# Kernel optimization log

Hardware: AMD Instinct MI355X
Metric: run time of the kernel (lower is better)

## Reference

```python
import jax, jax.numpy as jnp
import numpy as np
import math

B, P, C, D, H = 4, 2048, 512, 1024, 16
DH = D // H
EPS = 1e-6


def setup_inputs() -> dict:
    key = jax.random.key(0)
    ks = jax.random.split(key, 10)
    para = jax.random.normal(ks[0], (B, P, D), dtype=jnp.float32)
    cluster = jax.random.normal(ks[1], (B, C, D), dtype=jnp.float32)
    e = jax.random.uniform(ks[2], (B, P, C), dtype=jnp.float32)
    edge = jnp.where(e > 0.5, e, 0.0)
    s = 1.0 / math.sqrt(D)
    Wq = jax.random.uniform(ks[3], (D, D), jnp.float32, -s, s)
    bq = jnp.zeros((D,), jnp.float32)
    Wk = jax.random.uniform(ks[4], (D, D), jnp.float32, -s, s)
    bk = jnp.zeros((D,), jnp.float32)
    Wv = jax.random.uniform(ks[5], (D, D), jnp.float32, -s, s)
    bv = jnp.zeros((D,), jnp.float32)
    gamma = jnp.ones((D,), jnp.float32)
    beta = jnp.zeros((D,), jnp.float32)
    return {"para": para, "cluster": cluster, "edge": edge,
            "Wq": Wq, "bq": bq, "Wk": Wk, "bk": bk, "Wv": Wv, "bv": bv,
            "gamma": gamma, "beta": beta}


def reference(para, cluster, edge, Wq, bq, Wk, bk, Wv, bv, gamma, beta):
    # projections: [B, L, D] -> [B, H, L, DH]
    def shape(x):
        b, l, _ = x.shape
        return x.reshape(b, l, H, DH).transpose(0, 2, 1, 3)

    q = shape(para @ Wq + bq) / math.sqrt(DH)   # [B,H,P,DH]
    k = shape(cluster @ Wk + bk)                # [B,H,C,DH]
    v = shape(cluster @ Wv + bv)                # [B,H,C,DH]

    scores = jnp.einsum('bhpd,bhcd->bhpc', q, k)  # [B,H,P,C]
    mask = (edge > 0)[:, None, :, :]              # broadcast over heads
    scores = jnp.where(mask, scores, -1e18)
    attn = jax.nn.softmax(scores, axis=-1)
    attn = attn * edge[:, None, :, :]             # post-softmax edge weighting
    # dropout is identity at inference
    ctx = jnp.einsum('bhpc,bhcd->bhpd', attn, v)  # [B,H,P,DH]
    ctx = ctx.transpose(0, 2, 1, 3).reshape(B, P, D)
    # LayerNorm(model_dim), eps=1e-6
    mu = jnp.mean(ctx, axis=-1, keepdims=True)
    var = jnp.mean(jnp.square(ctx - mu), axis=-1, keepdims=True)
    out = (ctx - mu) * jax.lax.rsqrt(var + EPS) * gamma + beta
    return out
```

## Files before the change

### kernel.cpp

```cpp
#include <hip/hip_runtime.h>

#define BB 4
#define PP 2048
#define CCLUS 512
#define DD 1024
#define HH 16
#define DHH 64

typedef __attribute__((ext_vector_type(8))) short short8;
typedef __attribute__((ext_vector_type(4))) float floatx4;
typedef unsigned short u16;
typedef unsigned int u32;
typedef unsigned long long u64;

__device__ __forceinline__ float bf2f(u16 u) {
  union { u32 i; float f; } v; v.i = ((u32)u) << 16; return v.f;
}
__device__ __forceinline__ u16 f2bf(float f) {
  union { float f; u32 i; } v; v.f = f;
  u32 x = v.i;
  return (u16)((x + 0x7fffu + ((x >> 16) & 1u)) >> 16);
}
__device__ __forceinline__ u64 pack4(float a, float b, float c, float d) {
  return (u64)f2bf(a) | ((u64)f2bf(b) << 16) | ((u64)f2bf(c) << 32) | ((u64)f2bf(d) << 48);
}

__device__ __forceinline__ floatx4 mfma16(short8 a, short8 b, floatx4 c) {
  return __builtin_amdgcn_mfma_f32_16x16x32_bf16(a, b, c, 0, 0, 0);
}

__device__ __forceinline__ void gload_lds16(const u16* g, u16* l) {
  __builtin_amdgcn_global_load_lds(
      (const __attribute__((address_space(1))) u32*)g,
      (__attribute__((address_space(3))) u32*)l, 16, 0, 0);
}

__global__ __launch_bounds__(256) void prep_k(
    const float* __restrict__ para, const float* __restrict__ cluster,
    const float* __restrict__ Wq, const float* __restrict__ Wk, const float* __restrict__ Wv,
    u16* __restrict__ Ap, u16* __restrict__ Ac,
    u16* __restrict__ WqT, u16* __restrict__ WkT, u16* __restrict__ WvT) {
  const int tid = threadIdx.x;
  if (blockIdx.x < 3072) {
    __shared__ u16 tile[32][33];
    const int job = blockIdx.x;
    const int z = job >> 10;
    const int t = job & 1023;
    const int bx = t & 31, by = t >> 5;
    const float* src = (z == 0) ? Wq : (z == 1) ? Wk : Wv;
    u16* dst = (z == 0) ? WqT : (z == 1) ? WkT : WvT;
    const int c = tid & 31, r0 = tid >> 5;
#pragma unroll
    for (int rr = 0; rr < 4; rr++) {
      const int row = r0 + rr * 8;
      tile[row][c] = f2bf(src[(size_t)(by * 32 + row) * DD + bx * 32 + c]);
    }
    __syncthreads();
#pragma unroll
    for (int rr = 0; rr < 4; rr++) {
      const int row = r0 + rr * 8;
      dst[(size_t)(bx * 32 + row) * DD + by * 32 + c] = tile[c][row];
    }
  } else {
    const int NP4 = (BB * PP * DD) / 4;
    const int NC4 = (BB * CCLUS * DD) / 4;
    const int stride = 1024 * 256;
    for (int i = (blockIdx.x - 3072) * 256 + tid; i < NP4 + NC4; i += stride) {
      const float* src; u16* dst; int j;
      if (i < NP4) { src = para; dst = Ap; j = i; }
      else         { src = cluster; dst = Ac; j = i - NP4; }
      const float4 v = *(const float4*)(src + (size_t)j * 4);
      *(u64*)(dst + (size_t)j * 4) = pack4(v.x, v.y, v.z, v.w);
    }
  }
}

__global__ __launch_bounds__(256) void qkv_gemm5(
    const u16* __restrict__ Ap, const u16* __restrict__ Ac,
    const u16* __restrict__ WqT, const u16* __restrict__ WkT, const u16* __restrict__ WvT,
    const float* __restrict__ bq, const float* __restrict__ bk, const float* __restrict__ bv,
    u16* __restrict__ Qb, u16* __restrict__ Kp, u16* __restrict__ Vt) {
  const int bx = blockIdx.x;
  const u16* A; const u16* BT; const float* bias; float scale; int mt, mode;
  if (bx < 64)      { A = Ap; BT = WqT; bias = bq; scale = 0.18033688f; mt = bx;      mode = 0; }
  else if (bx < 80) { A = Ac; BT = WkT; bias = bk; scale = 1.0f;        mt = bx - 64; mode = 1; }
  else              { A = Ac; BT = WvT; bias = bv; scale = 1.0f;        mt = bx - 80; mode = 2; }

  __shared__ __align__(16) u16 SH[16384];
  u16* As = SH;
  u16* Bs = SH + 4096;
  u16* T2 = SH;

  const int tid = threadIdx.x;
  const int w = tid >> 6, lane = tid & 63, quad = lane >> 4, cidx = lane & 15;
  const int wy = w >> 1, wx = w & 1;
  const int m0 = mt * 128, n0 = blockIdx.y * 128;

  floatx4 acc[4][4];
#pragma unroll
  for (int i = 0; i < 4; i++)
#pragma unroll
    for (int j = 0; j < 4; j++) acc[i][j] = (floatx4){0.f, 0.f, 0.f, 0.f};

  const int row0 = tid >> 2, kc0 = tid & 3;
  const int offG0 = row0 * 1024 + kc0 * 8;
  const int offG1 = (row0 + 64) * 1024 + kc0 * 8;
  u16* ldsA0 = As + (size_t)(w * 64) * 8;
  u16* ldsA1 = As + (size_t)(w * 64 + 256) * 8;
  u16* ldsB0 = Bs + (size_t)(w * 64) * 8;
  u16* ldsB1 = Bs + (size_t)(w * 64 + 256) * 8;

  const u16* Abase = A + (size_t)m0 * 1024;
  const u16* Bbase = BT + (size_t)n0 * 1024;

  for (int kt = 0; kt < 32; kt++) {
    const u16* Ak = Abase + kt * 32;
    const u16* Bk = Bbase + kt * 32;
    gload_lds16(Ak + offG0, ldsA0);
    gload_lds16(Ak + offG1, ldsA1);
    gload_lds16(Bk + offG0, ldsB0);
    gload_lds16(Bk + offG1, ldsB1);
    __syncthreads();

    short8 af[4], bfr[4];
#pragma unroll
    for (int i = 0; i < 4; i++) {
      int ra = wy * 64 + i * 16 + cidx;
      af[i] = *(const short8*)&As[ra * 32 + quad * 8];
      int rb = wx * 64 + i * 16 + cidx;
      bfr[i] = *(const short8*)&Bs[rb * 32 + quad * 8];
    }
#pragma unroll
    for (int mi = 0; mi < 4; mi++)
#pragma unroll
      for (int ni = 0; ni < 4; ni++)
        acc[mi][ni] = mfma16(af[mi], bfr[ni], acc[mi][ni]);
    __syncthreads();
  }

  if (mode != 2) {
#pragma unroll
    for (int ni = 0; ni < 4; ni++) {
      const int ncol = n0 + wx * 64 + ni * 16 + cidx;
      const float bvv = bias[ncol];
#pragma unroll
      for (int mi = 0; mi < 4; mi++) {
        const int mrow = m0 + wy * 64 + mi * 16 + quad * 4;
        if (mode == 1) {
          const int hh2 = ncol >> 6, dh = ncol & 63;
#pragma unroll
          for (int r = 0; r < 4; r++) {
            const int row = mrow + r;
            const int bb = row >> 9, c = row & 511;
            Kp[((size_t)(bb * HH + hh2) * CCLUS + c) * DHH + dh] = f2bf(acc[mi][ni][r] + bvv);
          }
        } else {
#pragma unroll
          for (int r = 0; r < 4; r++) {
            float v = (acc[mi][ni][r] + bvv) * scale;
            Qb[(size_t)(mrow + r) * 1024 + ncol] = f2bf(v);
          }
        }
      }
    }
  } else {
    const int b = m0 >> 9;
    const int c0g = m0 & 511;
    const int h0g = n0 >> 6;
#pragma unroll
    for (int p = 0; p < 2; p++) {
      if (wx == p) {
#pragma unroll
        for (int ni = 0; ni < 4; ni++) {
          const int col = ni * 16 + cidx;
          const float bvv = bias[n0 + wx * 64 + col];
          const int swzv = (col & 7) << 3;
#pragma unroll
          for (int mi = 0; mi < 4; mi++) {
            const int rowb = wy * 64 + mi * 16 + quad * 4;
            *(u64*)&T2[col * 128 + (rowb ^ swzv)] =
                pack4(acc[mi][ni][0] + bvv, acc[mi][ni][1] + bvv,
                      acc[mi][ni][2] + bvv, acc[mi][ni][3] + bvv);
          }
        }
      }
      __syncthreads();
      {
        const int col = tid >> 2, quarter = tid & 3;
        const int swzv = (col & 7) << 3;
        u16* vrow = Vt + ((size_t)(b * HH + h0g + p) * 64 + col) * 512 + c0g + quarter * 32;
#pragma unroll
        for (int j = 0; j < 4; j++) {
          const short8 vv = *(const short8*)&T2[col * 128 + ((quarter * 32 + j * 8) ^ swzv)];
          *(short8*)(vrow + j * 8) = vv;
        }
      }
      __syncthreads();
    }
  }
}

__global__ __launch_bounds__(512, 8) void attn_k5(
    const u16* __restrict__ Qb, const u16* __restrict__ Kp, const u16* __restrict__ Vt,
    const float* __restrict__ edge, float* __restrict__ ctx) {
  const int b = blockIdx.z, h = blockIdx.y, p0 = blockIdx.x * 128;
  const int tid = threadIdx.x;
  const int w = tid >> 6, lane = tid & 63, quad = lane >> 4, cidx = lane & 15;

  __shared__ __align__(16) u16 Ks[2][64 * 64];
  __shared__ __align__(16) u16 Vs[2][64 * 64];

  const u16* __restrict__ Kbh = Kp + (size_t)(b * HH + h) * CCLUS * DHH;
  const u16* __restrict__ Vbh = Vt + (size_t)(b * HH + h) * DHH * CCLUS;

  const int prow = p0 + w * 16 + cidx;
  const u16* qg = Qb + (size_t)(b * PP + prow) * DD + h * DHH + quad * 8;
  const short8 qf0 = *(const short8*)qg;
  const short8 qf1 = *(const short8*)(qg + 32);
  const float* Erow = edge + (size_t)(b * PP + prow) * CCLUS;

  float srow = 0.f;
  floatx4 oacc[4];
#pragma unroll
  for (int nt = 0; nt < 4; nt++) oacc[nt] = (floatx4){0.f, 0.f, 0.f, 0.f};

  const int srow_i = tid >> 3;
  const int sc = ((tid & 7) ^ (srow_i & 7)) << 3;
  const int ldsoff = w * 512;

  auto STAGE = [&](int cc, int bufi) {
    const u16* kg = Kbh + (size_t)cc * 64 * DHH;
    const u16* vg = Vbh + cc * 64;
    gload_lds16(kg + (size_t)srow_i * DHH + sc, &Ks[bufi][ldsoff]);
    gload_lds16(vg + (size_t)srow_i * CCLUS + sc, &Vs[bufi][ldsoff]);
  };

  STAGE(0, 0);
  __syncthreads();

  const int swz = (cidx & 7) << 3;

  for (int cc = 0; cc < 8; cc++) {
    const int bufi = cc & 1;
    if (cc < 7) STAGE(cc + 1, bufi ^ 1);
    const u16* __restrict__ KsB = &Ks[bufi][0];
    const u16* __restrict__ VsB = &Vs[bufi][0];

#pragma unroll
    for (int ks = 0; ks < 2; ks++) {
      u32 pa[2], pb[2];
#pragma unroll
      for (int tt = 0; tt < 2; tt++) {
        const int t = ks * 2 + tt;
        const int krow = (t * 16 + cidx) * 64;
        const short8 kf0 = *(const short8*)&KsB[krow + ((quad * 8) ^ swz)];
        const short8 kf1 = *(const short8*)&KsB[krow + ((32 + quad * 8) ^ swz)];
        floatx4 s4 = (floatx4){0.f, 0.f, 0.f, 0.f};
        __builtin_amdgcn_s_setprio(1);
        s4 = mfma16(kf0, qf0, s4);
        s4 = mfma16(kf1, qf1, s4);
        __builtin_amdgcn_s_setprio(0);
        const int ce = cc * 64 + t * 16 + quad * 4;
        const float4 e4 = *(const float4*)(Erow + ce);
        float E[4];
#pragma unroll
        for (int r = 0; r < 4; r++) {
          const float e = (&e4.x)[r];
          float x = fminf(s4[r], 21.6f);
          float ex;
          asm("v_exp_f32 %0, %1\n\ts_nop 0" : "=v"(ex) : "v"(x));
          ex = (e > 0.f) ? ex : 0.f;
          srow += ex;
          E[r] = ex * e;
        }
        asm("v_cvt_pk_bf16_f32 %0, %1, %2" : "=v"(pa[tt]) : "v"(E[0]), "v"(E[1]));
        asm("v_cvt_pk_bf16_f32 %0, %1, %2" : "=v"(pb[tt]) : "v"(E[2]), "v"(E[3]));
      }
      asm("v_permlane32_swap_b32 %0, %1" : "+v"(pa[0]), "+v"(pa[1]));
      asm("v_permlane16_swap_b32 %0, %1" : "+v"(pa[0]), "+v"(pa[1]));
      asm("v_permlane32_swap_b32 %0, %1" : "+v"(pb[0]), "+v"(pb[1]));
      asm("v_permlane16_swap_b32 %0, %1" : "+v"(pb[0]), "+v"(pb[1]));
      union { u32 u[4]; short8 s; } af;
      af.u[0] = pa[0]; af.u[1] = pb[0]; af.u[2] = pa[1]; af.u[3] = pb[1];
      __builtin_amdgcn_s_setprio(1);
#pragma unroll
      for (int nt = 0; nt < 4; nt++) {
        const short8 bfr =
            *(const short8*)&VsB[(nt * 16 + cidx) * 64 + ((ks * 32 + quad * 8) ^ swz)];
        oacc[nt] = mfma16(af.s, bfr, oacc[nt]);
      }
      __builtin_amdgcn_s_setprio(0);
    }
    __syncthreads();
  }

  srow += __shfl_xor(srow, 16, 64);
  srow += __shfl_xor(srow, 32, 64);
  const float sinv = (srow > 0.f) ? 1.0f / srow : 0.f;

#pragma unroll
  for (int r = 0; r < 4; r++) {
    const float sv = __shfl(sinv, quad * 4 + r, 16);
#pragma unroll
    for (int nt = 0; nt < 4; nt++) {
      const size_t off =
          (size_t)(b * PP + p0 + w * 16 + quad * 4 + r) * DD + h * DHH + nt * 16 + cidx;
      ctx[off] = oacc[nt][r] * sv;
    }
  }
}

__global__ __launch_bounds__(256) void ln_k(
    float* buf, const float* __restrict__ gamma, const float* __restrict__ beta) {
  const int row = blockIdx.x, tid = threadIdx.x;
  const int w = tid >> 6, lane = tid & 63;
  float* x = buf + (size_t)row * DD + tid * 4;
  float4 v = *(const float4*)x;
  float s = v.x + v.y + v.z + v.w;
  float sq = v.x * v.x + v.y * v.y + v.z * v.z + v.w * v.w;
#pragma unroll
  for (int off = 1; off < 64; off <<= 1) {
    s += __shfl_xor(s, off, 64);
    sq += __shfl_xor(sq, off, 64);
  }
  __shared__ float red[8];
  if (lane == 0) { red[w] = s; red[4 + w] = sq; }
  __syncthreads();
  s = red[0] + red[1] + red[2] + red[3];
  sq = red[4] + red[5] + red[6] + red[7];
  const float mu = s * (1.f / 1024.f);
  const float var = sq * (1.f / 1024.f) - mu * mu;
  const float rs = rsqrtf(fmaxf(var, 0.f) + 1e-6f);
  const float4 gr = *(const float4*)(gamma + tid * 4);
  const float4 br = *(const float4*)(beta + tid * 4);
  float4 y;
  y.x = (v.x - mu) * rs * gr.x + br.x;
  y.y = (v.y - mu) * rs * gr.y + br.y;
  y.z = (v.z - mu) * rs * gr.z + br.z;
  y.w = (v.w - mu) * rs * gr.w + br.w;
  *(float4*)x = y;
}

extern "C" void kernel_launch(void* const* d_in, const int* in_sizes, int n_in,
                              void* d_out, int out_size, void* d_ws, size_t ws_size,
                              hipStream_t stream) {
  const float* para    = (const float*)d_in[0];
  const float* cluster = (const float*)d_in[1];
  const float* edge    = (const float*)d_in[2];
  const float* Wq      = (const float*)d_in[3];
  const float* bq      = (const float*)d_in[4];
  const float* Wk      = (const float*)d_in[5];
  const float* bk      = (const float*)d_in[6];
  const float* Wv      = (const float*)d_in[7];
  const float* bv      = (const float*)d_in[8];
  const float* gamma   = (const float*)d_in[9];
  const float* beta    = (const float*)d_in[10];
  float* out = (float*)d_out;

  u16* WqT = (u16*)d_ws;
  u16* WkT = WqT + (size_t)1024 * 1024;
  u16* WvT = WkT + (size_t)1024 * 1024;
  u16* Qb  = WvT + (size_t)1024 * 1024;
  u16* Kp  = Qb  + (size_t)8192 * 1024;
  u16* Vt  = Kp  + (size_t)2048 * 1024;
  u16* Ap  = Vt  + (size_t)2048 * 1024;
  u16* Ac  = Ap  + (size_t)8192 * 1024;

  prep_k<<<dim3(4096), dim3(256), 0, stream>>>(para, cluster, Wq, Wk, Wv,
                                               Ap, Ac, WqT, WkT, WvT);
  qkv_gemm5<<<dim3(96, 8), dim3(256), 0, stream>>>(Ap, Ac, WqT, WkT, WvT,
                                                   bq, bk, bv, Qb, Kp, Vt);
  attn_k5<<<dim3(PP / 128, HH, BB), dim3(512), 0, stream>>>(Qb, Kp, Vt, edge, out);
  ln_k<<<dim3(BB * PP), dim3(256), 0, stream>>>(out, gamma, beta);
}
```

Baseline: 231.0 us.

## Drop LDS staging in attention; load K/V fragments directly from global memory

The attention kernel no longer double-buffers K and V tiles through shared memory with async global-to-LDS loads and barriers. Each wave now reads its MFMA K and V fragments straight from global memory (through cache) in a flat 16-step loop, and the launch-bounds occupancy hint drops from 8 to 4. The aim is to remove the barriers and LDS traffic. The cost is redundant global/L2 reads, since all 8 waves of a block fetch the same K/V data, plus less latency hiding without explicit prefetch.

```diff
diff --git a/kernel.cpp b/kernel.cpp
--- a/kernel.cpp
+++ b/kernel.cpp
@@ -200,16 +200,13 @@
   }
 }
 
-__global__ __launch_bounds__(512, 8) void attn_k5(
+__global__ __launch_bounds__(512, 4) void attn_k10(
     const u16* __restrict__ Qb, const u16* __restrict__ Kp, const u16* __restrict__ Vt,
     const float* __restrict__ edge, float* __restrict__ ctx) {
   const int b = blockIdx.z, h = blockIdx.y, p0 = blockIdx.x * 128;
   const int tid = threadIdx.x;
   const int w = tid >> 6, lane = tid & 63, quad = lane >> 4, cidx = lane & 15;
 
-  __shared__ __align__(16) u16 Ks[2][64 * 64];
-  __shared__ __align__(16) u16 Vs[2][64 * 64];
-
   const u16* __restrict__ Kbh = Kp + (size_t)(b * HH + h) * CCLUS * DHH;
   const u16* __restrict__ Vbh = Vt + (size_t)(b * HH + h) * DHH * CCLUS;
 
@@ -219,79 +216,55 @@
   const short8 qf1 = *(const short8*)(qg + 32);
   const float* Erow = edge + (size_t)(b * PP + prow) * CCLUS;
 
+  const u16* kfp = Kbh + (size_t)cidx * DHH + quad * 8;
+  const u16* vfp = Vbh + (size_t)cidx * CCLUS + quad * 8;
+
   float srow = 0.f;
   floatx4 oacc[4];
 #pragma unroll
   for (int nt = 0; nt < 4; nt++) oacc[nt] = (floatx4){0.f, 0.f, 0.f, 0.f};
 
-  const int srow_i = tid >> 3;
-  const int sc = ((tid & 7) ^ (srow_i & 7)) << 3;
-  const int ldsoff = w * 512;
-
-  auto STAGE = [&](int cc, int bufi) {
-    const u16* kg = Kbh + (size_t)cc * 64 * DHH;
-    const u16* vg = Vbh + cc * 64;
-    gload_lds16(kg + (size_t)srow_i * DHH + sc, &Ks[bufi][ldsoff]);
-    gload_lds16(vg + (size_t)srow_i * CCLUS + sc, &Vs[bufi][ldsoff]);
-  };
-
-  STAGE(0, 0);
-  __syncthreads();
-
-  const int swz = (cidx & 7) << 3;
-
-  for (int cc = 0; cc < 8; cc++) {
-    const int bufi = cc & 1;
-    if (cc < 7) STAGE(cc + 1, bufi ^ 1);
-    const u16* __restrict__ KsB = &Ks[bufi][0];
-    const u16* __restrict__ VsB = &Vs[bufi][0];
-
-#pragma unroll
-    for (int ks = 0; ks < 2; ks++) {
-      u32 pa[2], pb[2];
-#pragma unroll
-      for (int tt = 0; tt < 2; tt++) {
-        const int t = ks * 2 + tt;
-        const int krow = (t * 16 + cidx) * 64;
-        const short8 kf0 = *(const short8*)&KsB[krow + ((quad * 8) ^ swz)];
-        const short8 kf1 = *(const short8*)&KsB[krow + ((32 + quad * 8) ^ swz)];
-        floatx4 s4 = (floatx4){0.f, 0.f, 0.f, 0.f};
-        __builtin_amdgcn_s_setprio(1);
-        s4 = mfma16(kf0, qf0, s4);
-        s4 = mfma16(kf1, qf1, s4);
-        __builtin_amdgcn_s_setprio(0);
-        const int ce = cc * 64 + t * 16 + quad * 4;
-        const float4 e4 = *(const float4*)(Erow + ce);
-        float E[4];
-#pragma unroll
-        for (int r = 0; r < 4; r++) {
-          const float e = (&e4.x)[r];
-          float x = fminf(s4[r], 21.6f);
-          float ex;
-          asm("v_exp_f32 %0, %1\n\ts_nop 0" : "=v"(ex) : "v"(x));
-          ex = (e > 0.f) ? ex : 0.f;
-          srow += ex;
-          E[r] = ex * e;
-        }
-        asm("v_cvt_pk_bf16_f32 %0, %1, %2" : "=v"(pa[tt]) : "v"(E[0]), "v"(E[1]));
-        asm("v_cvt_pk_bf16_f32 %0, %1, %2" : "=v"(pb[tt]) : "v"(E[2]), "v"(E[3]));
+#pragma unroll 2
+  for (int g = 0; g < 16; g++) {
+    u32 pa[2], pb[2];
+#pragma unroll
+    for (int tt = 0; tt < 2; tt++) {
+      const int ct = g * 2 + tt;
+      const short8 kf0 = *(const short8*)(kfp + ct * 1024);
+      const short8 kf1 = *(const short8*)(kfp + ct * 1024 + 32);
+      floatx4 s4 = (floatx4){0.f, 0.f, 0.f, 0.f};
+      __builtin_amdgcn_s_setprio(1);
+      s4 = mfma16(kf0, qf0, s4);
+      s4 = mfma16(kf1, qf1, s4);
+      __builtin_amdgcn_s_setprio(0);
+      const float4 e4 = *(const float4*)(Erow + ct * 16 + quad * 4);
+      float E[4];
+#pragma unroll
+      for (int r = 0; r < 4; r++) {
+        const float e = (&e4.x)[r];
+        float x = fminf(s4[r], 21.6f);
+        float ex;
+        asm("v_exp_f32 %0, %1\n\ts_nop 0" : "=v"(ex) : "v"(x));
+        ex = (e > 0.f) ? ex : 0.f;
+        srow += ex;
+        E[r] = ex * e;
       }
-      asm("v_permlane32_swap_b32 %0, %1" : "+v"(pa[0]), "+v"(pa[1]));
-      asm("v_permlane16_swap_b32 %0, %1" : "+v"(pa[0]), "+v"(pa[1]));
-      asm("v_permlane32_swap_b32 %0, %1" : "+v"(pb[0]), "+v"(pb[1]));
-      asm("v_permlane16_swap_b32 %0, %1" : "+v"(pb[0]), "+v"(pb[1]));
-      union { u32 u[4]; short8 s; } af;
-      af.u[0] = pa[0]; af.u[1] = pb[0]; af.u[2] = pa[1]; af.u[3] = pb[1];
-      __builtin_amdgcn_s_setprio(1);
-#pragma unroll
-      for (int nt = 0; nt < 4; nt++) {
-        const short8 bfr =
-            *(const short8*)&VsB[(nt * 16 + cidx) * 64 + ((ks * 32 + quad * 8) ^ swz)];
-        oacc[nt] = mfma16(af.s, bfr, oacc[nt]);
-      }
-      __builtin_amdgcn_s_setprio(0);
-    }
-    __syncthreads();
+      asm("v_cvt_pk_bf16_f32 %0, %1, %2" : "=v"(pa[tt]) : "v"(E[0]), "v"(E[1]));
+      asm("v_cvt_pk_bf16_f32 %0, %1, %2" : "=v"(pb[tt]) : "v"(E[2]), "v"(E[3]));
+    }
+    asm("v_permlane32_swap_b32 %0, %1" : "+v"(pa[0]), "+v"(pa[1]));
+    asm("v_permlane16_swap_b32 %0, %1" : "+v"(pa[0]), "+v"(pa[1]));
+    asm("v_permlane32_swap_b32 %0, %1" : "+v"(pb[0]), "+v"(pb[1]));
+    asm("v_permlane16_swap_b32 %0, %1" : "+v"(pb[0]), "+v"(pb[1]));
+    union { u32 u[4]; short8 s; } af;
+    af.u[0] = pa[0]; af.u[1] = pb[0]; af.u[2] = pa[1]; af.u[3] = pb[1];
+    __builtin_amdgcn_s_setprio(1);
+#pragma unroll
+    for (int nt = 0; nt < 4; nt++) {
+      const short8 vb = *(const short8*)(vfp + nt * 8192 + g * 32);
+      oacc[nt] = mfma16(af.s, vb, oacc[nt]);
+    }
+    __builtin_amdgcn_s_setprio(0);
   }
 
   srow += __shfl_xor(srow, 16, 64);
@@ -370,6 +343,6 @@
                                                Ap, Ac, WqT, WkT, WvT);
   qkv_gemm5<<<dim3(96, 8), dim3(256), 0, stream>>>(Ap, Ac, WqT, WkT, WvT,
                                                    bq, bk, bv, Qb, Kp, Vt);
-  attn_k5<<<dim3(PP / 128, HH, BB), dim3(512), 0, stream>>>(Qb, Kp, Vt, edge, out);
+  attn_k10<<<dim3(PP / 128, HH, BB), dim3(512), 0, stream>>>(Qb, Kp, Vt, edge, out);
   ln_k<<<dim3(BB * PP), dim3(256), 0, stream>>>(out, gamma, beta);
 }
```

After: 361.6 us. 1.57x slower.
